# Optimization experiments

Hardware: AMD Instinct MI355X
Metric: run time of the kernel (lower is better)

## Reference

```python
import jax, jax.numpy as jnp
import numpy as np

FEATURE_HEIGHT = 50
FEATURE_WIDTH = 50


def setup_inputs() -> dict:
    key = jax.random.key(0)
    k1, k2, k3 = jax.random.split(key, 3)
    bs, K, H, D = 16, FEATURE_HEIGHT * FEATURE_WIDTH, 8, 32
    Q, L, P = 2000, 1, 4
    value = jax.random.normal(k1, (bs, K, H, D), dtype=jnp.float32)
    value_spatial_shapes = jnp.array([[FEATURE_HEIGHT, FEATURE_WIDTH]], dtype=jnp.int64)
    sampling_locations = jax.random.uniform(k2, (bs, Q, H, L, P, 2), dtype=jnp.float32)
    attention_weights = jax.random.uniform(k3, (bs, Q, H, L, P), dtype=jnp.float32)
    return {
        "value": value,
        "value_spatial_shapes": value_spatial_shapes,
        "sampling_locations": sampling_locations,
        "attention_weights": attention_weights,
    }


def _bilinear_sample(img, grid):
    """torch.F.grid_sample(mode='bilinear', padding_mode='zeros', align_corners=False).

    img:  (N, D, h, w)
    grid: (N, Q, P, 2), last dim (x, y) in [-1, 1]
    returns (N, D, Q, P)
    """
    N, D, h, w = img.shape
    # unnormalize (align_corners=False)
    x = (grid[..., 0] + 1.0) * (w * 0.5) - 0.5  # (N, Q, P)
    y = (grid[..., 1] + 1.0) * (h * 0.5) - 0.5
    x0 = jnp.floor(x)
    y0 = jnp.floor(y)
    x1 = x0 + 1.0
    y1 = y0 + 1.0
    wx1 = x - x0
    wx0 = 1.0 - wx1
    wy1 = y - y0
    wy0 = 1.0 - wy1

    img_flat = img.reshape(N, D, h * w)

    def corner(ix, iy, wgt):
        valid = ((ix >= 0) & (ix < w) & (iy >= 0) & (iy < h)).astype(img.dtype)
        ixc = jnp.clip(ix, 0, w - 1).astype(jnp.int32)
        iyc = jnp.clip(iy, 0, h - 1).astype(jnp.int32)
        idx = (iyc * w + ixc).reshape(N, -1)  # (N, Q*P)
        vals = jnp.take_along_axis(img_flat, idx[:, None, :], axis=2)  # (N, D, Q*P)
        vals = vals.reshape(N, D, *ix.shape[1:])  # (N, D, Q, P)
        return vals * (wgt * valid)[:, None]

    out = corner(x0, y0, wx0 * wy0)
    out = out + corner(x1, y0, wx1 * wy0)
    out = out + corner(x0, y1, wx0 * wy1)
    out = out + corner(x1, y1, wx1 * wy1)
    return out


def reference(value, value_spatial_shapes, sampling_locations, attention_weights):
    bs, K, H, D = value.shape
    _, Q, _, L, P, _ = sampling_locations.shape
    h, w = FEATURE_HEIGHT, FEATURE_WIDTH

    sampling_grids = 2.0 * sampling_locations - 1.0  # (bs, Q, H, L, P, 2)
    # value -> (bs*H, D, h, w)
    v = value.reshape(bs, K, H * D).transpose(0, 2, 1).reshape(bs * H, D, h, w)
    # level 0 grid -> (bs*H, Q, P, 2)
    g = jnp.transpose(sampling_grids[:, :, :, 0], (0, 2, 1, 3, 4)).reshape(bs * H, Q, P, 2)
    sampled = _bilinear_sample(v, g)  # (bs*H, D, Q, P)
    # attention weights -> (bs*H, 1, Q, L*P)
    aw = jnp.transpose(attention_weights, (0, 2, 1, 3, 4)).reshape(bs * H, 1, Q, L * P)
    out = (sampled * aw).sum(-1)  # (bs*H, D, Q)
    out = out.reshape(bs, H * D, Q).transpose(0, 2, 1)  # (bs, Q, H*D)
    return out
```

## Files before the change

kernel.cpp:

```cpp
#include <hip/hip_runtime.h>


#define FH 50
#define FW 50
#define KK (FH * FW)
#define NH 8
#define ND 32
#define NQ 2000
#define NP 4

#define QPB 8
#define BLOCKS_PER_B (NQ / QPB)

__global__ __launch_bounds__(256, 2) void deform_attn_kernel(
    const float* __restrict__ value,
    const float* __restrict__ loc,
    const float* __restrict__ attw,
    float* __restrict__ out)
{
    const int x = blockIdx.x;
    const int xcd = x & 7;
    const int slot = x >> 3;
    const int phase = (slot >= BLOCKS_PER_B) ? 1 : 0;
    const int b = xcd + (phase << 3);
    const int q0 = (slot - phase * BLOCKS_PER_B) * QPB;

    const int t = threadIdx.x;
    const int c = t & 7;
    const int lg = t >> 3;
    const int h = lg & 7;
    const int qo = lg >> 3;

    const char* __restrict__ vb =
        (const char*)(value + (size_t)b * KK * NH * ND);
    const int hc = h * (ND * 4) + c * 16;

    const int qA = q0 + qo;
    const int gidA = (b * NQ + qA) * NH + h;

    float4 accA = {0.f, 0.f, 0.f, 0.f};
    float4 accB = {0.f, 0.f, 0.f, 0.f};

    auto sample = [&](int gid, float4& acc) {
        const float4* __restrict__ lp = (const float4*)loc + (size_t)gid * 2;
        const float4 l0 = lp[0];
        const float4 l1 = lp[1];
        const float4 a4 = ((const float4*)attw)[gid];

        const float pxx[NP] = {l0.x, l0.z, l1.x, l1.z};
        const float pyy[NP] = {l0.y, l0.w, l1.y, l1.w};
        const float awp[NP] = {a4.x, a4.y, a4.z, a4.w};

        unsigned offs[16];
        float wts[16];
#pragma unroll
        for (int p = 0; p < NP; ++p) {
            const float fx = pxx[p] * (float)FW - 0.5f;
            const float fy = pyy[p] * (float)FH - 0.5f;
            const float x0f = floorf(fx);
            const float y0f = floorf(fy);
            const int x0 = (int)x0f, y0 = (int)y0f;
            const int x1 = x0 + 1, y1 = y0 + 1;
            const float wx1 = fx - x0f, wx0 = 1.f - wx1;
            const float wy1 = fy - y0f, wy0 = 1.f - wy1;

            const bool vx0 = (x0 >= 0) & (x0 < FW);
            const bool vx1 = (x1 >= 0) & (x1 < FW);
            const bool vy0 = (y0 >= 0) & (y0 < FH);
            const bool vy1 = (y1 >= 0) & (y1 < FH);

            const int cx0 = min(max(x0, 0), FW - 1);
            const int cx1 = min(max(x1, 0), FW - 1);
            const int cy0 = min(max(y0, 0), FH - 1);
            const int cy1 = min(max(y1, 0), FH - 1);

            offs[p * 4 + 0] = (unsigned)((cy0 * FW + cx0) * 1024 + hc);
            offs[p * 4 + 1] = (unsigned)((cy0 * FW + cx1) * 1024 + hc);
            offs[p * 4 + 2] = (unsigned)((cy1 * FW + cx0) * 1024 + hc);
            offs[p * 4 + 3] = (unsigned)((cy1 * FW + cx1) * 1024 + hc);

            wts[p * 4 + 0] = ((vx0 & vy0) ? (wx0 * wy0) : 0.f) * awp[p];
            wts[p * 4 + 1] = ((vx1 & vy0) ? (wx1 * wy0) : 0.f) * awp[p];
            wts[p * 4 + 2] = ((vx0 & vy1) ? (wx0 * wy1) : 0.f) * awp[p];
            wts[p * 4 + 3] = ((vx1 & vy1) ? (wx1 * wy1) : 0.f) * awp[p];
        }

        float4 v[16];
#pragma unroll
        for (int i = 0; i < 16; ++i)
            v[i] = *(const float4*)(vb + offs[i]);
#pragma unroll
        for (int i = 0; i < 16; ++i) {
            acc.x += wts[i] * v[i].x;
            acc.y += wts[i] * v[i].y;
            acc.z += wts[i] * v[i].z;
            acc.w += wts[i] * v[i].w;
        }
    };

    sample(gidA, accA);
    sample(gidA + 4 * NH, accB);

    float4* __restrict__ op = (float4*)out;
    op[(size_t)(b * NQ + qA) * (NH * ND / 4) + h * (ND / 4) + c] = accA;
    op[(size_t)(b * NQ + qA + 4) * (NH * ND / 4) + h * (ND / 4) + c] = accB;
}

extern "C" void kernel_launch(void* const* d_in, const int* in_sizes, int n_in,
                              void* d_out, int out_size, void* d_ws, size_t ws_size,
                              hipStream_t stream) {
    const float* value = (const float*)d_in[0];
    const float* loc  = (const float*)d_in[2];
    const float* attw = (const float*)d_in[3];
    float* out = (float*)d_out;

    const int blocks = 16 * BLOCKS_PER_B;
    deform_attn_kernel<<<blocks, 256, 0, stream>>>(value, loc, attw, out);
}
```

Measured before the change: 118.3 us.

## Stage per-head value channel slices in LDS as fp16 for bilinear gathers

```diff
diff --git a/kernel.cpp b/kernel.cpp
--- a/kernel.cpp
+++ b/kernel.cpp
@@ -1,4 +1,5 @@
 #include <hip/hip_runtime.h>
+#include <hip/hip_fp16.h>
 
 
 #define FH 50
@@ -8,50 +9,61 @@
 #define ND 32
 #define NQ 2000
 #define NP 4
+#define QHALF 1000
 
-#define QPB 8
-#define BLOCKS_PER_B (NQ / QPB)
-
-__global__ __launch_bounds__(256, 2) void deform_attn_kernel(
+__global__ __launch_bounds__(256, 4) void deform_attn_kernel(
     const float* __restrict__ value,
     const float* __restrict__ loc,
     const float* __restrict__ attw,
     float* __restrict__ out)
 {
-    const int x = blockIdx.x;
-    const int xcd = x & 7;
-    const int slot = x >> 3;
-    const int phase = (slot >= BLOCKS_PER_B) ? 1 : 0;
-    const int b = xcd + (phase << 3);
-    const int q0 = (slot - phase * BLOCKS_PER_B) * QPB;
+    const int blk = blockIdx.x;
+    const int xcd = blk & 7;
+    const int s = blk >> 3;
+    const int cg = s >> 5;
+    const int t5 = s & 31;
+    const int bph = t5 >> 4;
+    const int h = (t5 >> 1) & 7;
+    const int qh = t5 & 1;
+    const int b = xcd + (bph << 3);
 
-    const int t = threadIdx.x;
-    const int c = t & 7;
-    const int lg = t >> 3;
-    const int h = lg & 7;
-    const int qo = lg >> 3;
+    __shared__ ushort sv[KK * 8];
+    {
+        const float4* __restrict__ vsrc = (const float4*)value;
+        const size_t vbase = (size_t)b * KK * 64 + h * 8 + cg * 2;
+        for (int i = threadIdx.x; i < 2 * KK; i += 256) {
+            const int k = i >> 1;
+            const int halfsel = i & 1;
+            const float4 f = vsrc[vbase + (size_t)k * 64 + halfsel];
+            const __half2 p0 = __floats2half2_rn(f.x, f.y);
+            const __half2 p1 = __floats2half2_rn(f.z, f.w);
+            uint2 packed;
+            packed.x = *(const unsigned int*)&p0;
+            packed.y = *(const unsigned int*)&p1;
+            *((uint2*)&sv[k * 8 + halfsel * 4]) = packed;
+        }
+    }
+    __syncthreads();
 
-    const char* __restrict__ vb =
-        (const char*)(value + (size_t)b * KK * NH * ND);
-    const int hc = h * (ND * 4) + c * 16;
+    const float4* __restrict__ loc4 = (const float4*)loc;
+    const float4* __restrict__ attw4 = (const float4*)attw;
+    float4* __restrict__ out4 = (float4*)out;
 
-    const int qA = q0 + qo;
-    const int gidA = (b * NQ + qA) * NH + h;
+    for (int r = 0; r < 4; ++r) {
+        const int ql = r * 256 + threadIdx.x;
+        if (ql >= QHALF) break;
+        const int q = qh * QHALF + ql;
+        const int gid = (b * NQ + q) * NH + h;
 
-    float4 accA = {0.f, 0.f, 0.f, 0.f};
-    float4 accB = {0.f, 0.f, 0.f, 0.f};
-
-    auto sample = [&](int gid, float4& acc) {
-        const float4* __restrict__ lp = (const float4*)loc + (size_t)gid * 2;
-        const float4 l0 = lp[0];
-        const float4 l1 = lp[1];
-        const float4 a4 = ((const float4*)attw)[gid];
+        const float4 l0 = loc4[(size_t)gid * 2];
+        const float4 l1 = loc4[(size_t)gid * 2 + 1];
+        const float4 a4 = attw4[gid];
 
         const float pxx[NP] = {l0.x, l0.z, l1.x, l1.z};
         const float pyy[NP] = {l0.y, l0.w, l1.y, l1.w};
         const float awp[NP] = {a4.x, a4.y, a4.z, a4.w};
 
-        unsigned offs[16];
+        int offs[16];
         float wts[16];
 #pragma unroll
         for (int p = 0; p < NP; ++p) {
@@ -74,10 +86,10 @@
             const int cy0 = min(max(y0, 0), FH - 1);
             const int cy1 = min(max(y1, 0), FH - 1);
 
-            offs[p * 4 + 0] = (unsigned)((cy0 * FW + cx0) * 1024 + hc);
-            offs[p * 4 + 1] = (unsigned)((cy0 * FW + cx1) * 1024 + hc);
-            offs[p * 4 + 2] = (unsigned)((cy1 * FW + cx0) * 1024 + hc);
-            offs[p * 4 + 3] = (unsigned)((cy1 * FW + cx1) * 1024 + hc);
+            offs[p * 4 + 0] = (cy0 * FW + cx0) * 8;
+            offs[p * 4 + 1] = (cy0 * FW + cx1) * 8;
+            offs[p * 4 + 2] = (cy1 * FW + cx0) * 8;
+            offs[p * 4 + 3] = (cy1 * FW + cx1) * 8;
 
             wts[p * 4 + 0] = ((vx0 & vy0) ? (wx0 * wy0) : 0.f) * awp[p];
             wts[p * 4 + 1] = ((vx1 & vy0) ? (wx1 * wy0) : 0.f) * awp[p];
@@ -85,25 +97,26 @@
             wts[p * 4 + 3] = ((vx1 & vy1) ? (wx1 * wy1) : 0.f) * awp[p];
         }
 
-        float4 v[16];
-#pragma unroll
-        for (int i = 0; i < 16; ++i)
-            v[i] = *(const float4*)(vb + offs[i]);
+        float a0 = 0.f, a1 = 0.f, a2 = 0.f, a3 = 0.f;
+        float a4_ = 0.f, a5 = 0.f, a6 = 0.f, a7 = 0.f;
 #pragma unroll
         for (int i = 0; i < 16; ++i) {
-            acc.x += wts[i] * v[i].x;
-            acc.y += wts[i] * v[i].y;
-            acc.z += wts[i] * v[i].z;
-            acc.w += wts[i] * v[i].w;
+            const uint4 rv = *((const uint4*)&sv[offs[i]]);
+            const float w = wts[i];
+            const float2 f0 = __half22float2(*(const __half2*)&rv.x);
+            const float2 f1 = __half22float2(*(const __half2*)&rv.y);
+            const float2 f2 = __half22float2(*(const __half2*)&rv.z);
+            const float2 f3 = __half22float2(*(const __half2*)&rv.w);
+            a0 += w * f0.x; a1 += w * f0.y;
+            a2 += w * f1.x; a3 += w * f1.y;
+            a4_ += w * f2.x; a5 += w * f2.y;
+            a6 += w * f3.x; a7 += w * f3.y;
         }
-    };
 
-    sample(gidA, accA);
-    sample(gidA + 4 * NH, accB);
-
-    float4* __restrict__ op = (float4*)out;
-    op[(size_t)(b * NQ + qA) * (NH * ND / 4) + h * (ND / 4) + c] = accA;
-    op[(size_t)(b * NQ + qA + 4) * (NH * ND / 4) + h * (ND / 4) + c] = accB;
+        const size_t o = (size_t)(b * NQ + q) * 64 + h * 8 + cg * 2;
+        out4[o] = make_float4(a0, a1, a2, a3);
+        out4[o + 1] = make_float4(a4_, a5, a6, a7);
+    }
 }
 
 extern "C" void kernel_launch(void* const* d_in, const int* in_sizes, int n_in,
@@ -114,6 +127,5 @@
     const float* attw = (const float*)d_in[3];
     float* out = (float*)d_out;
 
-    const int blocks = 16 * BLOCKS_PER_B;
-    deform_attn_kernel<<<blocks, 256, 0, stream>>>(value, loc, attw, out);
+    deform_attn_kernel<<<1024, 256, 0, stream>>>(value, loc, attw, out);
 }
```

Result: slower. 129.3 us (+9.2%).
